# Performance work log

Measured on AMD Instinct MI355X. Metric: run time of the kernel, lower is better.

Reference implementation:

```python
import jax, jax.numpy as jnp
import numpy as np
import math

N_LEVELS = 4          # quadtree depth; leaves = 4**4 = 256
N_HEAD = 8
LN_EPS = 1e-5

def _tree_consts():
    # level d has 4**d nodes; offsets[d] = first node index of level d
    sizes = [4 ** d for d in range(N_LEVELS + 1)]
    offsets = np.concatenate([[0], np.cumsum(sizes)])
    n_nodes = int(offsets[-1])  # 341
    parent = np.full(n_nodes, -1, np.int64)
    for d in range(1, N_LEVELS + 1):
        idx = offsets[d] + np.arange(sizes[d])
        parent[idx] = offsets[d - 1] + np.arange(sizes[d]) // 4
    # chain[c, k] = k-th ancestor of c (k=0 -> self); padded by clamping at root
    chain = np.zeros((n_nodes, N_LEVELS + 1), np.int64)
    chain[:, 0] = np.arange(n_nodes)
    for k in range(1, N_LEVELS + 1):
        prev = chain[:, k - 1]
        chain[:, k] = np.where(parent[prev] >= 0, parent[prev], prev)
    nodes_at = [offsets[d] + np.arange(sizes[d]) for d in range(N_LEVELS + 1)]
    return chain, nodes_at, n_nodes

CHAIN, NODES_AT, N_NODES = _tree_consts()

def layernorm(x, g, b):
    m = jnp.mean(x, -1, keepdims=True)
    v = jnp.var(x, -1, keepdims=True)
    return (x - m) * jax.lax.rsqrt(v + LN_EPS) * g + b

def mhsa(x, w_qkv, b_qkv, w_proj, b_proj):
    B, N, E = x.shape
    hd = E // N_HEAD
    qkv = x @ w_qkv + b_qkv                       # (B, N, 3E)
    q, k, v = jnp.split(qkv, 3, axis=-1)
    sh = lambda t: t.reshape(B, N, N_HEAD, hd).transpose(0, 2, 1, 3)  # (B,H,N,hd)
    q, k, v = sh(q), sh(k), sh(v)
    att = jax.nn.softmax(jnp.einsum('bhqd,bhkd->bhqk', q, k) / math.sqrt(hd), axis=-1)
    o = jnp.einsum('bhqk,bhkd->bhqd', att, v).transpose(0, 2, 1, 3).reshape(B, N, E)
    return o @ w_proj + b_proj

def branch_mlp(x, M, b1, w2, b2):
    # Sparse equivalent of einsum('bni,bjmni->bmj', x, W1): W1[:, c, a, :]
    # is nonzero only for a in {c} U ancestors(c), with the weight matrix
    # depending only on (depth(c), depth(a)). Group nodes by depth and sum
    # over ancestor offsets k (depth(a) = d - k).
    B, N, E = x.shape
    h = jnp.zeros((B, N, 4 * E), x.dtype)
    for d in range(N_LEVELS + 1):
        nd = NODES_AT[d]                           # static numpy indices
        acc = jnp.zeros((B, nd.shape[0], 4 * E), x.dtype)
        for k in range(d + 1):
            src = CHAIN[nd, k]                     # ancestor at depth d-k
            acc = acc + jnp.einsum('bne,je->bnj', x[:, src, :], M[d, d - k])
        h = h.at[:, nd, :].set(acc)
    h = jax.nn.relu(h + b1[None, :, :])
    return h @ w2 + b2

def setup_inputs() -> dict:
    key = jax.random.key(0)
    ks = jax.random.split(key, 6)
    B, N, E = 64, N_NODES, 512
    s = 0.02
    return {
        'x': jax.random.normal(ks[0], (B, N, E), jnp.float32),
        'ln1_g': jnp.ones((E,), jnp.float32),
        'ln1_b': jnp.zeros((E,), jnp.float32),
        'w_qkv': jax.random.normal(ks[1], (E, 3 * E), jnp.float32) * s,
        'b_qkv': jnp.zeros((3 * E,), jnp.float32),
        'w_proj': jax.random.normal(ks[2], (E, E), jnp.float32) * s,
        'b_proj': jnp.zeros((E,), jnp.float32),
        'ln2_g': jnp.ones((E,), jnp.float32),
        'ln2_b': jnp.zeros((E,), jnp.float32),
        'mlp_M': jax.random.normal(ks[3], (N_LEVELS + 1, N_LEVELS + 1, 4 * E, E), jnp.float32) * s,
        'mlp_b1': jnp.zeros((N, 4 * E), jnp.float32),
        'w2': jax.random.normal(ks[4], (4 * E, E), jnp.float32) * s,
        'b2': jnp.zeros((E,), jnp.float32),
    }

def reference(x, ln1_g, ln1_b, w_qkv, b_qkv, w_proj, b_proj,
              ln2_g, ln2_b, mlp_M, mlp_b1, w2, b2):
    x = x + mhsa(layernorm(x, ln1_g, ln1_b), w_qkv, b_qkv, w_proj, b_proj)
    x = x + branch_mlp(layernorm(x, ln2_g, ln2_b), mlp_M, mlp_b1, w2, b2)
    return x
```

## Files before the change

kernel.cpp:

```cpp
#include <hip/hip_runtime.h>
#include <hip/hip_bf16.h>


typedef __attribute__((ext_vector_type(8))) __bf16 bf16x8;
typedef __attribute__((ext_vector_type(4))) float f32x4;
typedef __attribute__((ext_vector_type(4))) unsigned int u32x4;

#define GF_RELU    1
#define GF_OUTBF16 2

static __device__ __forceinline__ bf16x8 bzero8() {
    u32x4 z = {0u, 0u, 0u, 0u};
    return __builtin_bit_cast(bf16x8, z);
}

__global__ void transpose_bf16_kernel(const float* __restrict__ in,
                                      __hip_bfloat16* __restrict__ out,
                                      int K, int N, int log2K) {
    int idx = blockIdx.x * 256 + threadIdx.x;
    if (idx >= K * N) return;
    int n = idx >> log2K;
    int k = idx & (K - 1);
    out[idx] = __float2bfloat16(in[(size_t)k * N + n]);
}

__global__ void pack_wcat_kernel(const float* __restrict__ M,
                                 __hip_bfloat16* __restrict__ out) {
    int p = blockIdx.y;
    int s, d;
    if (p < 5)       { s = 0; d = p; }
    else if (p < 9)  { s = 1; d = p - 4; }
    else if (p < 12) { s = 2; d = p - 7; }
    else if (p < 14) { s = 3; d = p - 9; }
    else             { s = 4; d = 4; }
    const int base_lut[5] = {0, 5, 9, 12, 14};
    size_t idx = (size_t)blockIdx.x * 256 + threadIdx.x;
    const size_t MB = 2048ull * 512;
    out[(size_t)base_lut[s] * MB + (size_t)(d - s) * MB + idx] =
        __float2bfloat16(M[((size_t)d * 5 + s) * MB + idx]);
}

__global__ __launch_bounds__(256) void ln_kernel(const float* __restrict__ x,
                                                 const float* __restrict__ g,
                                                 const float* __restrict__ b,
                                                 __hip_bfloat16* __restrict__ out) {
    int tok = blockIdx.x;
    const float* xr = x + (size_t)tok * 512;
    int t = threadIdx.x;
    float v0 = xr[t], v1 = xr[t + 256];
    float s = v0 + v1;
    float s2 = v0 * v0 + v1 * v1;
    #pragma unroll
    for (int o = 32; o > 0; o >>= 1) {
        s  += __shfl_down(s, o);
        s2 += __shfl_down(s2, o);
    }
    __shared__ float ps[4], ps2[4];
    int w = t >> 6, lane = t & 63;
    if (lane == 0) { ps[w] = s; ps2[w] = s2; }
    __syncthreads();
    if (t == 0) {
        float ts = 0.f, ts2 = 0.f;
        #pragma unroll
        for (int i = 0; i < 4; i++) { ts += ps[i]; ts2 += ps2[i]; }
        ps[0] = ts * (1.f / 512.f);
        ps2[0] = ts2 * (1.f / 512.f);
    }
    __syncthreads();
    float m = ps[0];
    float var = ps2[0] - m * m;
    float r = rsqrtf(var + 1e-5f);
    out[(size_t)tok * 512 + t]       = __float2bfloat16((v0 - m) * r * g[t] + b[t]);
    out[(size_t)tok * 512 + t + 256] = __float2bfloat16((v1 - m) * r * g[t + 256] + b[t + 256]);
}

#define ATT_STR 72
__global__ __launch_bounds__(256) void attn_mfma_kernel(const __hip_bfloat16* __restrict__ qkv,
                                                        __hip_bfloat16* __restrict__ ctx) {
    __shared__ __bf16 kt_lds[64 * ATT_STR];
    __shared__ __bf16 vt_lds[64 * ATT_STR];
    __shared__ __bf16 pbuf[4 * 48 * ATT_STR];

    const int bh = blockIdx.x;
    const int half = blockIdx.y;
    const int b = bh >> 3, h = bh & 7;
    const int tid = threadIdx.x;
    const int w = tid >> 6, lane = tid & 63;
    const int q = lane >> 4, l16 = lane & 15;
    const int rowbase = half * 192 + w * 48;
    __bf16* pw = pbuf + w * 48 * ATT_STR;

    bf16x8 qf[3][2];
    #pragma unroll
    for (int mi = 0; mi < 3; mi++) {
        int row = rowbase + mi * 16 + l16;
        #pragma unroll
        for (int ks = 0; ks < 2; ks++) {
            if (row < 341)
                qf[mi][ks] = *(const bf16x8*)(qkv + (size_t)(b * 341 + row) * 1536 +
                                              h * 64 + ks * 32 + q * 8);
            else
                qf[mi][ks] = bzero8();
        }
    }

    f32x4 O[3][4];
    float mrun[3][4], lrun[3][4];
    #pragma unroll
    for (int mi = 0; mi < 3; mi++) {
        #pragma unroll
        for (int ni = 0; ni < 4; ni++) { f32x4 z = {0.f,0.f,0.f,0.f}; O[mi][ni] = z; }
        #pragma unroll
        for (int rr = 0; rr < 4; rr++) { mrun[mi][rr] = -1e30f; lrun[mi][rr] = 0.f; }
    }

    for (int kt6 = 0; kt6 < 6; kt6++) {
        const int kbase = kt6 * 64;
        __syncthreads();
        {
            int key = tid >> 2, kg = tid & 3;
            int gk = kbase + key;
            bf16x8 a0 = bzero8(), a1 = bzero8();
            if (gk < 341) {
                const __hip_bfloat16* src =
                    qkv + (size_t)(b * 341 + gk) * 1536 + 512 + h * 64 + kg * 16;
                a0 = *(const bf16x8*)src;
                a1 = *(const bf16x8*)(src + 8);
            }
            *(bf16x8*)(kt_lds + key * ATT_STR + kg * 16)     = a0;
            *(bf16x8*)(kt_lds + key * ATT_STR + kg * 16 + 8) = a1;
        }
        {
            int key = tid & 63, dg = tid >> 6;
            int gk = kbase + key;
            bf16x8 a0 = bzero8(), a1 = bzero8();
            if (gk < 341) {
                const __hip_bfloat16* src =
                    qkv + (size_t)(b * 341 + gk) * 1536 + 1024 + h * 64 + dg * 16;
                a0 = *(const bf16x8*)src;
                a1 = *(const bf16x8*)(src + 8);
            }
            #pragma unroll
            for (int j = 0; j < 8; j++) {
                vt_lds[(dg * 16 + j) * ATT_STR + key]     = a0[j];
                vt_lds[(dg * 16 + 8 + j) * ATT_STR + key] = a1[j];
            }
        }
        __syncthreads();

        f32x4 S[3][4];
        #pragma unroll
        for (int mi = 0; mi < 3; mi++)
            #pragma unroll
            for (int ni = 0; ni < 4; ni++) { f32x4 z = {0.f,0.f,0.f,0.f}; S[mi][ni] = z; }
        #pragma unroll
        for (int ks = 0; ks < 2; ks++) {
            bf16x8 bf_[4];
            #pragma unroll
            for (int ni = 0; ni < 4; ni++)
                bf_[ni] = *(const bf16x8*)(kt_lds + (ni * 16 + l16) * ATT_STR + ks * 32 + q * 8);
            #pragma unroll
            for (int mi = 0; mi < 3; mi++)
                #pragma unroll
                for (int ni = 0; ni < 4; ni++)
                    S[mi][ni] = __builtin_amdgcn_mfma_f32_16x16x32_bf16(qf[mi][ks], bf_[ni],
                                                                        S[mi][ni], 0, 0, 0);
        }

        float cmask[4];
        #pragma unroll
        for (int ni = 0; ni < 4; ni++)
            cmask[ni] = (kbase + ni * 16 + l16 < 341) ? 0.f : -1e30f;

        #pragma unroll
        for (int mi = 0; mi < 3; mi++) {
            #pragma unroll
            for (int rr = 0; rr < 4; rr++) {
                float rmax = -1e30f;
                #pragma unroll
                for (int ni = 0; ni < 4; ni++)
                    rmax = fmaxf(rmax, fmaf(S[mi][ni][rr], 0.125f, cmask[ni]));
                rmax = fmaxf(rmax, __shfl_xor(rmax, 1));
                rmax = fmaxf(rmax, __shfl_xor(rmax, 2));
                rmax = fmaxf(rmax, __shfl_xor(rmax, 4));
                rmax = fmaxf(rmax, __shfl_xor(rmax, 8));
                float mnew = fmaxf(mrun[mi][rr], rmax);
                float alpha = __expf(mrun[mi][rr] - mnew);
                mrun[mi][rr] = mnew;
                float psum = 0.f;
                #pragma unroll
                for (int ni = 0; ni < 4; ni++) {
                    float p = __expf(fmaf(S[mi][ni][rr], 0.125f, cmask[ni]) - mnew);
                    S[mi][ni][rr] = p;
                    psum += p;
                    O[mi][ni][rr] *= alpha;
                }
                psum += __shfl_xor(psum, 1);
                psum += __shfl_xor(psum, 2);
                psum += __shfl_xor(psum, 4);
                psum += __shfl_xor(psum, 8);
                lrun[mi][rr] = lrun[mi][rr] * alpha + psum;
            }
            #pragma unroll
            for (int ni = 0; ni < 4; ni++)
                #pragma unroll
                for (int rr = 0; rr < 4; rr++)
                    pw[(mi * 16 + q * 4 + rr) * ATT_STR + ni * 16 + l16] =
                        (__bf16)S[mi][ni][rr];
        }
        __syncthreads();

        #pragma unroll
        for (int ks = 0; ks < 2; ks++) {
            bf16x8 pf[3], vf[4];
            #pragma unroll
            for (int mi = 0; mi < 3; mi++)
                pf[mi] = *(const bf16x8*)(pw + (mi * 16 + l16) * ATT_STR + ks * 32 + q * 8);
            #pragma unroll
            for (int ni = 0; ni < 4; ni++)
                vf[ni] = *(const bf16x8*)(vt_lds + (ni * 16 + l16) * ATT_STR + ks * 32 + q * 8);
            #pragma unroll
            for (int mi = 0; mi < 3; mi++)
                #pragma unroll
                for (int ni = 0; ni < 4; ni++)
                    O[mi][ni] = __builtin_amdgcn_mfma_f32_16x16x32_bf16(pf[mi], vf[ni],
                                                                        O[mi][ni], 0, 0, 0);
        }
    }

    #pragma unroll
    for (int mi = 0; mi < 3; mi++) {
        #pragma unroll
        for (int rr = 0; rr < 4; rr++) {
            int row = rowbase + mi * 16 + q * 4 + rr;
            if (row >= 341) continue;
            float inv = 1.f / lrun[mi][rr];
            __hip_bfloat16* op = ctx + (size_t)(b * 341 + row) * 512 + h * 64;
            #pragma unroll
            for (int ni = 0; ni < 4; ni++)
                op[ni * 16 + l16] = __float2bfloat16(O[mi][ni][rr] * inv);
        }
    }
}

template <bool GATHER>
__global__ __launch_bounds__(256) void gemm_bf16(
    const __hip_bfloat16* __restrict__ A, const __hip_bfloat16* __restrict__ Bt,
    const float* __restrict__ bias, const float* __restrict__ resid,
    float* __restrict__ Cf, __hip_bfloat16* __restrict__ Cb,
    int Mrows, int N, int K, int flags, int depth) {
    __shared__ __hip_bfloat16 As[128 * 32];
    __shared__ __hip_bfloat16 Bs[128 * 32];
    const int tid = threadIdx.x;
    const int r = tid >> 1;
    const int kh = (tid & 1) << 4;
    const int gr = blockIdx.x * 128 + r;
    const int gn = blockIdx.y * 128 + r;
    const int lane = tid & 63;
    const int w = tid >> 6;
    const int wm = (w >> 1) << 6;
    const int wn = (w & 1) << 6;
    const int q = lane >> 4;
    const int l16 = lane & 15;

    size_t abase;
    if (GATHER) {
        const int dsh = depth << 1;
        const int bmask = (1 << dsh) - 1;
        int b = gr >> dsh;
        int i = gr & bmask;
        int node = (0x55555555 & bmask) + i;
        abase = ((size_t)(b * 341 + node)) << 9;
    } else {
        abase = (size_t)gr * K;
    }

    f32x4 acc[4][4];
    #pragma unroll
    for (int i = 0; i < 4; i++)
        #pragma unroll
        for (int j = 0; j < 4; j++) {
            f32x4 z = {0.f, 0.f, 0.f, 0.f};
            acc[i][j] = z;
        }

    for (int k0 = 0; k0 < K; k0 += 32) {
        bf16x8 va0 = bzero8(), va1 = bzero8(), vb0, vb1;
        if (gr < Mrows) {
            const bf16x8* p = (const bf16x8*)(A + abase + k0 + kh);
            va0 = p[0];
            va1 = p[1];
        }
        {
            const bf16x8* p = (const bf16x8*)(Bt + (size_t)gn * K + k0 + kh);
            vb0 = p[0];
            vb1 = p[1];
        }
        __syncthreads();
        *(bf16x8*)(As + r * 32 + kh)     = va0;
        *(bf16x8*)(As + r * 32 + kh + 8) = va1;
        *(bf16x8*)(Bs + r * 32 + kh)     = vb0;
        *(bf16x8*)(Bs + r * 32 + kh + 8) = vb1;
        __syncthreads();
        bf16x8 af[4], bfr[4];
        #pragma unroll
        for (int mi = 0; mi < 4; mi++)
            af[mi] = *(const bf16x8*)(As + (wm + mi * 16 + l16) * 32 + q * 8);
        #pragma unroll
        for (int ni = 0; ni < 4; ni++)
            bfr[ni] = *(const bf16x8*)(Bs + (wn + ni * 16 + l16) * 32 + q * 8);
        #pragma unroll
        for (int mi = 0; mi < 4; mi++)
            #pragma unroll
            for (int ni = 0; ni < 4; ni++)
                acc[mi][ni] = __builtin_amdgcn_mfma_f32_16x16x32_bf16(
                    af[mi], bfr[ni], acc[mi][ni], 0, 0, 0);
    }

    #pragma unroll
    for (int mi = 0; mi < 4; mi++) {
        #pragma unroll
        for (int rr = 0; rr < 4; rr++) {
            int grow = blockIdx.x * 128 + wm + mi * 16 + q * 4 + rr;
            if (grow >= Mrows) continue;
            size_t obase = (size_t)grow * N;
            #pragma unroll
            for (int ni = 0; ni < 4; ni++) {
                int col = blockIdx.y * 128 + wn + ni * 16 + l16;
                float v = acc[mi][ni][rr];
                if (bias) v += bias[col];
                if (resid) v += resid[obase + col];
                if (flags & GF_RELU) v = fmaxf(v, 0.f);
                if (flags & GF_OUTBF16)
                    Cb[obase + col] = __float2bfloat16(v);
                else
                    Cf[obase + col] = v;
            }
        }
    }
}

__global__ __launch_bounds__(256) void combine_kernel(const __hip_bfloat16* __restrict__ Y,
                                                      const float* __restrict__ b1,
                                                      __hip_bfloat16* __restrict__ h) {
    const size_t yoff[5] = {0, 655360, 2752512, 9043968, 25821184};
    int row = blockIdx.x;
    int b = row / 341;
    int node = row - b * 341;
    int d = (node >= 85) ? 4 : (node >= 21) ? 3 : (node >= 5) ? 2 : (node >= 1) ? 1 : 0;
    int i = node - (0x55555555 & ((1 << (d << 1)) - 1));
    int j = threadIdx.x << 3;

    float acc[8];
    const float* bp = b1 + (size_t)node * 2048 + j;
    f32x4 b0 = *(const f32x4*)bp;
    f32x4 b4 = *(const f32x4*)(bp + 4);
    #pragma unroll
    for (int u = 0; u < 4; u++) { acc[u] = b0[u]; acc[u + 4] = b4[u]; }

    #pragma unroll
    for (int s = 0; s < 5; s++) {
        if (s <= d) {
            int a = i >> ((d - s) << 1);
            int width = (5 - s) << 11;
            const bf16x8 v = *(const bf16x8*)(Y + yoff[s] +
                (size_t)((b << (s << 1)) + a) * width + ((d - s) << 11) + j);
            #pragma unroll
            for (int u = 0; u < 8; u++) acc[u] += (float)v[u];
        }
    }
    bf16x8 o;
    #pragma unroll
    for (int u = 0; u < 8; u++) o[u] = (__bf16)fmaxf(acc[u], 0.f);
    *(bf16x8*)(h + (size_t)row * 2048 + j) = o;
}

extern "C" void kernel_launch(void* const* d_in, const int* in_sizes, int n_in,
                              void* d_out, int out_size, void* d_ws, size_t ws_size,
                              hipStream_t stream) {
    const float* x      = (const float*)d_in[0];
    const float* ln1_g  = (const float*)d_in[1];
    const float* ln1_b  = (const float*)d_in[2];
    const float* w_qkv  = (const float*)d_in[3];
    const float* b_qkv  = (const float*)d_in[4];
    const float* w_proj = (const float*)d_in[5];
    const float* b_proj = (const float*)d_in[6];
    const float* ln2_g  = (const float*)d_in[7];
    const float* ln2_b  = (const float*)d_in[8];
    const float* mlp_M  = (const float*)d_in[9];
    const float* mlp_b1 = (const float*)d_in[10];
    const float* w2     = (const float*)d_in[11];
    const float* b2     = (const float*)d_in[12];
    float* out = (float*)d_out;

    const int M = 64 * 341;

    char* ws = (char*)d_ws;
    size_t off = 0;
    auto alloc = [&](size_t bytes) -> char* {
        char* p = ws + off;
        off += (bytes + 255) & ~(size_t)255;
        return p;
    };
    __hip_bfloat16* xn     = (__hip_bfloat16*)alloc((size_t)M * 512 * 2);
    __hip_bfloat16* wqkvT  = (__hip_bfloat16*)alloc(1536ull * 512 * 2);
    __hip_bfloat16* wprojT = (__hip_bfloat16*)alloc(512ull * 512 * 2);
    __hip_bfloat16* w2T    = (__hip_bfloat16*)alloc(512ull * 2048 * 2);
    __hip_bfloat16* wcat   = (__hip_bfloat16*)alloc(15ull * 2048 * 512 * 2);
    __hip_bfloat16* hbuf   = (__hip_bfloat16*)alloc((size_t)M * 2048 * 2);
    const size_t qkv_bytes = (size_t)M * 1536 * 2;
    const size_t y_bytes   = 59375616ull * 2;
    char* shared = alloc(y_bytes);
    __hip_bfloat16* qkv = (__hip_bfloat16*)shared;
    __hip_bfloat16* ctx = (__hip_bfloat16*)(shared + qkv_bytes);
    __hip_bfloat16* Y   = (__hip_bfloat16*)shared;
    if (off > ws_size) return;

    transpose_bf16_kernel<<<(512 * 1536 + 255) / 256, 256, 0, stream>>>(w_qkv, wqkvT, 512, 1536, 9);
    transpose_bf16_kernel<<<(512 * 512 + 255) / 256, 256, 0, stream>>>(w_proj, wprojT, 512, 512, 9);
    transpose_bf16_kernel<<<(2048 * 512 + 255) / 256, 256, 0, stream>>>(w2, w2T, 2048, 512, 11);
    pack_wcat_kernel<<<dim3(4096, 15), 256, 0, stream>>>(mlp_M, wcat);

    ln_kernel<<<M, 256, 0, stream>>>(x, ln1_g, ln1_b, xn);
    gemm_bf16<false><<<dim3((M + 127) / 128, 1536 / 128), 256, 0, stream>>>(
        xn, wqkvT, b_qkv, nullptr, nullptr, qkv, M, 1536, 512, GF_OUTBF16, 0);
    attn_mfma_kernel<<<dim3(512, 2), 256, 0, stream>>>(qkv, ctx);
    gemm_bf16<false><<<dim3((M + 127) / 128, 512 / 128), 256, 0, stream>>>(
        ctx, wprojT, b_proj, x, out, nullptr, M, 512, 512, 0, 0);

    ln_kernel<<<M, 256, 0, stream>>>(out, ln2_g, ln2_b, xn);
    const size_t yoff[5]     = {0, 655360, 2752512, 9043968, 25821184};
    const size_t wcat_off[5] = {0, 5, 9, 12, 14};
    for (int s = 0; s <= 4; s++) {
        int rows = 64 << (2 * s);
        int Ns = (5 - s) * 2048;
        gemm_bf16<true><<<dim3((rows + 127) / 128, Ns / 128), 256, 0, stream>>>(
            xn, wcat + wcat_off[s] * (2048ull * 512), nullptr, nullptr, nullptr,
            Y + yoff[s], rows, Ns, 512, GF_OUTBF16, s);
    }
    combine_kernel<<<M, 256, 0, stream>>>(Y, mlp_b1, hbuf);
    gemm_bf16<false><<<dim3((M + 127) / 128, 512 / 128), 256, 0, stream>>>(
        hbuf, w2T, b2, out, out, nullptr, M, 512, 2048, 0, 0);
}
```

Baseline: 858.0 us.

## Replace 128x128 GEMM with pipelined 256x256 LDS-DMA kernel with XCD remap

Replaces the simple register-staged 128x128 bf16 GEMM with a 256x256-tile, 512-thread kernel. It loads tiles directly into double-buffered, XOR-swizzled LDS using global_load_lds, and interleaves those loads with MFMA phases under explicit barriers and priority hints. A 1D grid with XCD-aware block remapping is meant to improve L2 locality. The goals are higher MFMA utilisation, fewer LDS bank conflicts and less global-load latency on all the GEMMs. The cost is 128KB of LDS per block and large tiles that may waste work on small-M gather stages, such as the 64-row depth-0 stage.

```diff
diff --git a/kernel.cpp b/kernel.cpp
--- a/kernel.cpp
+++ b/kernel.cpp
@@ -243,91 +243,198 @@
     }
 }
 
+__device__ __forceinline__ void gload16(const __hip_bfloat16* g, __bf16* l) {
+    __builtin_amdgcn_global_load_lds(
+        (const __attribute__((address_space(1))) void*)g,
+        (__attribute__((address_space(3))) void*)l, 16, 0, 0);
+}
+
+#define FULL_BAR() do { asm volatile("" ::: "memory");                        \
+    __builtin_amdgcn_sched_barrier(0);                                        \
+    __builtin_amdgcn_s_barrier();                                             \
+    __builtin_amdgcn_sched_barrier(0); } while (0)
+
+#define LGKM0() do {                                                          \
+    asm volatile("s_waitcnt lgkmcnt(0)" ::: "memory");                        \
+    __builtin_amdgcn_sched_barrier(0); } while (0)
+
+#define STAGE(arr, pr, isB, h, koff) do {                                     \
+    __bf16* _d = &smem[((((((pr) << 1) + (isB)) << 1) + (h)) << 13) + w * 1024]; \
+    gload16(arr[h][0] + (koff), _d);                                          \
+    gload16(arr[h][1] + (koff), _d + 512);                                    \
+} while (0)
+
 template <bool GATHER>
-__global__ __launch_bounds__(256) void gemm_bf16(
+__global__ __launch_bounds__(512, 2) void gemm256(
     const __hip_bfloat16* __restrict__ A, const __hip_bfloat16* __restrict__ Bt,
     const float* __restrict__ bias, const float* __restrict__ resid,
     float* __restrict__ Cf, __hip_bfloat16* __restrict__ Cb,
-    int Mrows, int N, int K, int flags, int depth) {
-    __shared__ __hip_bfloat16 As[128 * 32];
-    __shared__ __hip_bfloat16 Bs[128 * 32];
+    int Mrows, int N, int K, int flags, int depth, int gridN) {
+    __shared__ __align__(128) __bf16 smem[65536];
+
+    const int nwg = gridDim.x;
+    const int bid = blockIdx.x;
+    const int xcd = bid & 7, o = bid >> 3;
+    const int qq = nwg >> 3, rr = nwg & 7;
+    const int lin = (xcd < rr ? xcd * (qq + 1) : rr * (qq + 1) + (xcd - rr) * qq) + o;
+    const int bx = lin / gridN;
+    const int by = lin - bx * gridN;
+    const int bm0 = bx << 8, bn0 = by << 8;
+
     const int tid = threadIdx.x;
-    const int r = tid >> 1;
-    const int kh = (tid & 1) << 4;
-    const int gr = blockIdx.x * 128 + r;
-    const int gn = blockIdx.y * 128 + r;
-    const int lane = tid & 63;
-    const int w = tid >> 6;
-    const int wm = (w >> 1) << 6;
-    const int wn = (w & 1) << 6;
-    const int q = lane >> 4;
-    const int l16 = lane & 15;
-
-    size_t abase;
-    if (GATHER) {
-        const int dsh = depth << 1;
-        const int bmask = (1 << dsh) - 1;
-        int b = gr >> dsh;
-        int i = gr & bmask;
-        int node = (0x55555555 & bmask) + i;
-        abase = ((size_t)(b * 341 + node)) << 9;
-    } else {
-        abase = (size_t)gr * K;
-    }
-
-    f32x4 acc[4][4];
-    #pragma unroll
-    for (int i = 0; i < 4; i++)
+    const int w = tid >> 6, l = tid & 63;
+    const int l16 = l & 15, q = l >> 4;
+    const int wm = w >> 2, wn = w & 3;
+    const int lr8 = l >> 3;
+    const int slog = (l & 7) ^ lr8;
+
+    const __hip_bfloat16* aptr[2][2];
+    const __hip_bfloat16* bptr[2][2];
+    #pragma unroll
+    for (int h = 0; h < 2; h++)
+        #pragma unroll
+        for (int j = 0; j < 2; j++) {
+            int lr = (w * 2 + j) * 8 + lr8;
+            int grow = bm0 + h * 128 + lr;
+            if (grow > Mrows - 1) grow = Mrows - 1;
+            size_t abase;
+            if (GATHER) {
+                const int dsh = depth << 1;
+                const int bmask = (1 << dsh) - 1;
+                int bb = grow >> dsh;
+                int ii = grow & bmask;
+                int node = (0x55555555 & bmask) + ii;
+                abase = ((size_t)(bb * 341 + node)) << 9;
+            } else {
+                abase = (size_t)grow * K;
+            }
+            aptr[h][j] = A + abase + slog * 8;
+            bptr[h][j] = Bt + (size_t)(bn0 + h * 128 + lr) * K + slog * 8;
+        }
+
+    const int sl0 = ((q ^ (l16 & 7)) << 3);
+    const int sl1 = (((4 + q) ^ (l16 & 7)) << 3);
+
+    f32x4 acc[8][4];
+    #pragma unroll
+    for (int i = 0; i < 8; i++)
         #pragma unroll
         for (int j = 0; j < 4; j++) {
             f32x4 z = {0.f, 0.f, 0.f, 0.f};
             acc[i][j] = z;
         }
 
-    for (int k0 = 0; k0 < K; k0 += 32) {
-        bf16x8 va0 = bzero8(), va1 = bzero8(), vb0, vb1;
-        if (gr < Mrows) {
-            const bf16x8* p = (const bf16x8*)(A + abase + k0 + kh);
-            va0 = p[0];
-            va1 = p[1];
-        }
-        {
-            const bf16x8* p = (const bf16x8*)(Bt + (size_t)gn * K + k0 + kh);
-            vb0 = p[0];
-            vb1 = p[1];
-        }
-        __syncthreads();
-        *(bf16x8*)(As + r * 32 + kh)     = va0;
-        *(bf16x8*)(As + r * 32 + kh + 8) = va1;
-        *(bf16x8*)(Bs + r * 32 + kh)     = vb0;
-        *(bf16x8*)(Bs + r * 32 + kh + 8) = vb1;
-        __syncthreads();
-        bf16x8 af[4], bfr[4];
-        #pragma unroll
-        for (int mi = 0; mi < 4; mi++)
-            af[mi] = *(const bf16x8*)(As + (wm + mi * 16 + l16) * 32 + q * 8);
-        #pragma unroll
-        for (int ni = 0; ni < 4; ni++)
-            bfr[ni] = *(const bf16x8*)(Bs + (wn + ni * 16 + l16) * 32 + q * 8);
-        #pragma unroll
-        for (int mi = 0; mi < 4; mi++)
-            #pragma unroll
-            for (int ni = 0; ni < 4; ni++)
-                acc[mi][ni] = __builtin_amdgcn_mfma_f32_16x16x32_bf16(
-                    af[mi], bfr[ni], acc[mi][ni], 0, 0, 0);
-    }
-
-    #pragma unroll
-    for (int mi = 0; mi < 4; mi++) {
-        #pragma unroll
-        for (int rr = 0; rr < 4; rr++) {
-            int grow = blockIdx.x * 128 + wm + mi * 16 + q * 4 + rr;
+    STAGE(aptr, 0, 0, 0, 0);  STAGE(aptr, 0, 0, 1, 0);
+    STAGE(bptr, 0, 1, 0, 0);  STAGE(bptr, 0, 1, 1, 0);
+    STAGE(bptr, 1, 1, 0, 64); STAGE(bptr, 1, 1, 1, 64);
+    STAGE(aptr, 1, 0, 0, 64); STAGE(aptr, 1, 0, 1, 64);
+    asm volatile("s_waitcnt vmcnt(8)" ::: "memory");
+    __builtin_amdgcn_sched_barrier(0);
+    FULL_BAR();
+
+    const int NT = K >> 6;
+    bf16x8 af[4][2], b0[2][2], b1[2][2];
+
+    for (int t = 0; t < NT; ++t) {
+        const int p = t & 1;
+        const int aro = ((p << 2) + wm) << 13;
+        const int bro = ((((p << 1) + 1) << 1) + (wn >> 1)) * 8192 + ((wn & 1) << 12);
+
+        #pragma unroll
+        for (int mi = 0; mi < 4; mi++) {
+            af[mi][0] = *(const bf16x8*)&smem[aro + (mi * 16 + l16) * 64 + sl0];
+            af[mi][1] = *(const bf16x8*)&smem[aro + (mi * 16 + l16) * 64 + sl1];
+        }
+        #pragma unroll
+        for (int ni = 0; ni < 2; ni++) {
+            b0[ni][0] = *(const bf16x8*)&smem[bro + (ni * 16 + l16) * 64 + sl0];
+            b0[ni][1] = *(const bf16x8*)&smem[bro + (ni * 16 + l16) * 64 + sl1];
+        }
+        if (t >= 1 && t + 1 < NT) STAGE(aptr, (t + 1) & 1, 0, 0, (t + 1) << 6);
+        FULL_BAR();
+        LGKM0();
+        __builtin_amdgcn_s_setprio(1);
+        #pragma unroll
+        for (int ks = 0; ks < 2; ks++)
+            #pragma unroll
+            for (int mi = 0; mi < 4; mi++)
+                #pragma unroll
+                for (int ni = 0; ni < 2; ni++)
+                    acc[mi][ni] = __builtin_amdgcn_mfma_f32_16x16x32_bf16(
+                        af[mi][ks], b0[ni][ks], acc[mi][ni], 0, 0, 0);
+        __builtin_amdgcn_s_setprio(0);
+        FULL_BAR();
+
+        #pragma unroll
+        for (int ni = 0; ni < 2; ni++) {
+            b1[ni][0] = *(const bf16x8*)&smem[bro + ((ni + 2) * 16 + l16) * 64 + sl0];
+            b1[ni][1] = *(const bf16x8*)&smem[bro + ((ni + 2) * 16 + l16) * 64 + sl1];
+        }
+        if (t >= 1 && t + 1 < NT) STAGE(aptr, (t + 1) & 1, 0, 1, (t + 1) << 6);
+        FULL_BAR();
+        LGKM0();
+        __builtin_amdgcn_s_setprio(1);
+        #pragma unroll
+        for (int ks = 0; ks < 2; ks++)
+            #pragma unroll
+            for (int mi = 0; mi < 4; mi++)
+                #pragma unroll
+                for (int ni = 0; ni < 2; ni++)
+                    acc[mi][ni + 2] = __builtin_amdgcn_mfma_f32_16x16x32_bf16(
+                        af[mi][ks], b1[ni][ks], acc[mi][ni + 2], 0, 0, 0);
+        __builtin_amdgcn_s_setprio(0);
+        FULL_BAR();
+
+        #pragma unroll
+        for (int mi = 0; mi < 4; mi++) {
+            af[mi][0] = *(const bf16x8*)&smem[aro + ((mi + 4) * 16 + l16) * 64 + sl0];
+            af[mi][1] = *(const bf16x8*)&smem[aro + ((mi + 4) * 16 + l16) * 64 + sl1];
+        }
+        if (t + 2 < NT) STAGE(bptr, p, 1, 0, (t + 2) << 6);
+        FULL_BAR();
+        LGKM0();
+        __builtin_amdgcn_s_setprio(1);
+        #pragma unroll
+        for (int ks = 0; ks < 2; ks++)
+            #pragma unroll
+            for (int mi = 0; mi < 4; mi++)
+                #pragma unroll
+                for (int ni = 0; ni < 2; ni++)
+                    acc[mi + 4][ni + 2] = __builtin_amdgcn_mfma_f32_16x16x32_bf16(
+                        af[mi][ks], b1[ni][ks], acc[mi + 4][ni + 2], 0, 0, 0);
+        __builtin_amdgcn_s_setprio(0);
+        FULL_BAR();
+
+        if (t + 2 < NT) STAGE(bptr, p, 1, 1, (t + 2) << 6);
+        __builtin_amdgcn_s_setprio(1);
+        #pragma unroll
+        for (int ks = 0; ks < 2; ks++)
+            #pragma unroll
+            for (int mi = 0; mi < 4; mi++)
+                #pragma unroll
+                for (int ni = 0; ni < 2; ni++)
+                    acc[mi + 4][ni] = __builtin_amdgcn_mfma_f32_16x16x32_bf16(
+                        af[mi][ks], b0[ni][ks], acc[mi + 4][ni], 0, 0, 0);
+        __builtin_amdgcn_s_setprio(0);
+        if (t + 1 < NT) {
+            if (t + 2 < NT) { asm volatile("s_waitcnt vmcnt(4)" ::: "memory"); }
+            else            { asm volatile("s_waitcnt vmcnt(0)" ::: "memory"); }
+            __builtin_amdgcn_sched_barrier(0);
+        }
+        FULL_BAR();
+    }
+
+    #pragma unroll
+    for (int mi = 0; mi < 8; mi++) {
+        #pragma unroll
+        for (int rr2 = 0; rr2 < 4; rr2++) {
+            int grow = bm0 + wm * 128 + mi * 16 + q * 4 + rr2;
             if (grow >= Mrows) continue;
             size_t obase = (size_t)grow * N;
             #pragma unroll
             for (int ni = 0; ni < 4; ni++) {
-                int col = blockIdx.y * 128 + wn + ni * 16 + l16;
-                float v = acc[mi][ni][rr];
+                int col = bn0 + wn * 64 + ni * 16 + l16;
+                float v = acc[mi][ni][rr2];
                 if (bias) v += bias[col];
                 if (resid) v += resid[obase + col];
                 if (flags & GF_RELU) v = fmaxf(v, 0.f);
@@ -416,17 +523,27 @@
     __hip_bfloat16* Y   = (__hip_bfloat16*)shared;
     if (off > ws_size) return;
 
+    auto g256 = [&](bool gather, const __hip_bfloat16* A, const __hip_bfloat16* Bt,
+                    const float* bias, const float* resid, float* Cf,
+                    __hip_bfloat16* Cb, int Mr, int N, int K, int flags, int depth) {
+        int gm = (Mr + 255) >> 8, gn = N >> 8;
+        if (gather)
+            gemm256<true><<<dim3(gm * gn), 512, 0, stream>>>(
+                A, Bt, bias, resid, Cf, Cb, Mr, N, K, flags, depth, gn);
+        else
+            gemm256<false><<<dim3(gm * gn), 512, 0, stream>>>(
+                A, Bt, bias, resid, Cf, Cb, Mr, N, K, flags, depth, gn);
+    };
+
     transpose_bf16_kernel<<<(512 * 1536 + 255) / 256, 256, 0, stream>>>(w_qkv, wqkvT, 512, 1536, 9);
     transpose_bf16_kernel<<<(512 * 512 + 255) / 256, 256, 0, stream>>>(w_proj, wprojT, 512, 512, 9);
     transpose_bf16_kernel<<<(2048 * 512 + 255) / 256, 256, 0, stream>>>(w2, w2T, 2048, 512, 11);
     pack_wcat_kernel<<<dim3(4096, 15), 256, 0, stream>>>(mlp_M, wcat);
 
     ln_kernel<<<M, 256, 0, stream>>>(x, ln1_g, ln1_b, xn);
-    gemm_bf16<false><<<dim3((M + 127) / 128, 1536 / 128), 256, 0, stream>>>(
-        xn, wqkvT, b_qkv, nullptr, nullptr, qkv, M, 1536, 512, GF_OUTBF16, 0);
+    g256(false, xn, wqkvT, b_qkv, nullptr, nullptr, qkv, M, 1536, 512, GF_OUTBF16, 0);
     attn_mfma_kernel<<<dim3(512, 2), 256, 0, stream>>>(qkv, ctx);
-    gemm_bf16<false><<<dim3((M + 127) / 128, 512 / 128), 256, 0, stream>>>(
-        ctx, wprojT, b_proj, x, out, nullptr, M, 512, 512, 0, 0);
+    g256(false, ctx, wprojT, b_proj, x, out, nullptr, M, 512, 512, 0, 0);
 
     ln_kernel<<<M, 256, 0, stream>>>(out, ln2_g, ln2_b, xn);
     const size_t yoff[5]     = {0, 655360, 2752512, 9043968, 25821184};
@@ -434,11 +551,9 @@
     for (int s = 0; s <= 4; s++) {
         int rows = 64 << (2 * s);
         int Ns = (5 - s) * 2048;
-        gemm_bf16<true><<<dim3((rows + 127) / 128, Ns / 128), 256, 0, stream>>>(
-            xn, wcat + wcat_off[s] * (2048ull * 512), nullptr, nullptr, nullptr,
-            Y + yoff[s], rows, Ns, 512, GF_OUTBF16, s);
+        g256(true, xn, wcat + wcat_off[s] * (2048ull * 512), nullptr, nullptr, nullptr,
+             Y + yoff[s], rows, Ns, 512, GF_OUTBF16, s);
     }
     combine_kernel<<<M, 256, 0, stream>>>(Y, mlp_b1, hbuf);
-    gemm_bf16<false><<<dim3((M + 127) / 128, 512 / 128), 256, 0, stream>>>(
-        hbuf, w2T, b2, out, out, nullptr, M, 512, 2048, 0, 0);
-}
+    g256(false, hbuf, w2T, b2, out, out, nullptr, M, 512, 2048, 0, 0);
+}
```

After: 918.7 us. +7.1%, slower.

## Fuse per-depth branch GEMMs into one launch and remap blocks across XCDs

Applied to the files above, without the earlier changes.

The five per-depth branch GEMM launches become a single grouped GEMM kernel. It uses a flat grid and picks the depth segment from the linear block index, so small depth-0/1 GEMMs no longer run as separate under-filled launches. All GEMMs now use a 1D grid with an XCD-aware block remap, so consecutive tiles sharing A/B rows land on the same XCD and its L2. This adds integer division and branching per block, and the block-to-tile ordering changes.

```diff
diff --git a/kernel.cpp b/kernel.cpp
--- a/kernel.cpp
+++ b/kernel.cpp
@@ -244,18 +244,17 @@
 }
 
 template <bool GATHER>
-__global__ __launch_bounds__(256) void gemm_bf16(
+static __device__ __forceinline__ void gemm128_body(
+    __hip_bfloat16* As, __hip_bfloat16* Bs,
     const __hip_bfloat16* __restrict__ A, const __hip_bfloat16* __restrict__ Bt,
     const float* __restrict__ bias, const float* __restrict__ resid,
     float* __restrict__ Cf, __hip_bfloat16* __restrict__ Cb,
-    int Mrows, int N, int K, int flags, int depth) {
-    __shared__ __hip_bfloat16 As[128 * 32];
-    __shared__ __hip_bfloat16 Bs[128 * 32];
+    int Mrows, int N, int K, int flags, int depth, int bm0, int bn0) {
     const int tid = threadIdx.x;
     const int r = tid >> 1;
     const int kh = (tid & 1) << 4;
-    const int gr = blockIdx.x * 128 + r;
-    const int gn = blockIdx.y * 128 + r;
+    const int gr = bm0 + r;
+    const int gn = bn0 + r;
     const int lane = tid & 63;
     const int w = tid >> 6;
     const int wm = (w >> 1) << 6;
@@ -321,12 +320,12 @@
     for (int mi = 0; mi < 4; mi++) {
         #pragma unroll
         for (int rr = 0; rr < 4; rr++) {
-            int grow = blockIdx.x * 128 + wm + mi * 16 + q * 4 + rr;
+            int grow = bm0 + wm + mi * 16 + q * 4 + rr;
             if (grow >= Mrows) continue;
             size_t obase = (size_t)grow * N;
             #pragma unroll
             for (int ni = 0; ni < 4; ni++) {
-                int col = blockIdx.y * 128 + wn + ni * 16 + l16;
+                int col = bn0 + wn + ni * 16 + l16;
                 float v = acc[mi][ni][rr];
                 if (bias) v += bias[col];
                 if (resid) v += resid[obase + col];
@@ -338,6 +337,53 @@
             }
         }
     }
+}
+
+static __device__ __forceinline__ int xcd_remap(int bid, int nwg) {
+    const int xcd = bid & 7, o = bid >> 3;
+    const int qq = nwg >> 3, rr = nwg & 7;
+    return (xcd < rr ? xcd * (qq + 1) : rr * (qq + 1) + (xcd - rr) * qq) + o;
+}
+
+__global__ __launch_bounds__(256) void gemm128(
+    const __hip_bfloat16* __restrict__ A, const __hip_bfloat16* __restrict__ Bt,
+    const float* __restrict__ bias, const float* __restrict__ resid,
+    float* __restrict__ Cf, __hip_bfloat16* __restrict__ Cb,
+    int Mrows, int N, int K, int flags, int gridN) {
+    __shared__ __hip_bfloat16 As[128 * 32];
+    __shared__ __hip_bfloat16 Bs[128 * 32];
+    const int lin = xcd_remap(blockIdx.x, gridDim.x);
+    const int bx = lin / gridN;
+    const int by = lin - bx * gridN;
+    gemm128_body<false>(As, Bs, A, Bt, bias, resid, Cf, Cb,
+                        Mrows, N, K, flags, 0, bx << 7, by << 7);
+}
+
+__global__ __launch_bounds__(256) void gemm_branch_fused(
+    const __hip_bfloat16* __restrict__ xn, const __hip_bfloat16* __restrict__ wcat,
+    __hip_bfloat16* __restrict__ Y) {
+    __shared__ __hip_bfloat16 As[128 * 32];
+    __shared__ __hip_bfloat16 Bs[128 * 32];
+    const int lin = xcd_remap(blockIdx.x, gridDim.x);
+    int s;
+    if (lin < 80)        s = 0;
+    else if (lin < 208)  s = 1;
+    else if (lin < 592)  s = 2;
+    else if (lin < 1616) s = 3;
+    else                 s = 4;
+    const int base_tab[5] = {0, 80, 208, 592, 1616};
+    const int gn_tab[5]   = {80, 64, 48, 32, 16};
+    const size_t yoff[5]  = {0, 655360, 2752512, 9043968, 25821184};
+    const int wcat_off[5] = {0, 5, 9, 12, 14};
+    const int loc = lin - base_tab[s];
+    const int gn = gn_tab[s];
+    const int bx = loc / gn;
+    const int by = loc - bx * gn;
+    const int Mrows = 64 << (s << 1);
+    const int N = (5 - s) << 11;
+    gemm128_body<true>(As, Bs, xn, wcat + (size_t)wcat_off[s] * (2048ull * 512),
+                       nullptr, nullptr, nullptr, Y + yoff[s],
+                       Mrows, N, 512, GF_OUTBF16, s, bx << 7, by << 7);
 }
 
 __global__ __launch_bounds__(256) void combine_kernel(const __hip_bfloat16* __restrict__ Y,
@@ -416,29 +462,26 @@
     __hip_bfloat16* Y   = (__hip_bfloat16*)shared;
     if (off > ws_size) return;
 
+    auto g128 = [&](const __hip_bfloat16* A, const __hip_bfloat16* Bt,
+                    const float* bias, const float* resid, float* Cf,
+                    __hip_bfloat16* Cb, int Mr, int N, int K, int flags) {
+        int gm = (Mr + 127) >> 7, gn = N >> 7;
+        gemm128<<<dim3(gm * gn), 256, 0, stream>>>(
+            A, Bt, bias, resid, Cf, Cb, Mr, N, K, flags, gn);
+    };
+
     transpose_bf16_kernel<<<(512 * 1536 + 255) / 256, 256, 0, stream>>>(w_qkv, wqkvT, 512, 1536, 9);
     transpose_bf16_kernel<<<(512 * 512 + 255) / 256, 256, 0, stream>>>(w_proj, wprojT, 512, 512, 9);
     transpose_bf16_kernel<<<(2048 * 512 + 255) / 256, 256, 0, stream>>>(w2, w2T, 2048, 512, 11);
     pack_wcat_kernel<<<dim3(4096, 15), 256, 0, stream>>>(mlp_M, wcat);
 
     ln_kernel<<<M, 256, 0, stream>>>(x, ln1_g, ln1_b, xn);
-    gemm_bf16<false><<<dim3((M + 127) / 128, 1536 / 128), 256, 0, stream>>>(
-        xn, wqkvT, b_qkv, nullptr, nullptr, qkv, M, 1536, 512, GF_OUTBF16, 0);
+    g128(xn, wqkvT, b_qkv, nullptr, nullptr, qkv, M, 1536, 512, GF_OUTBF16);
     attn_mfma_kernel<<<dim3(512, 2), 256, 0, stream>>>(qkv, ctx);
-    gemm_bf16<false><<<dim3((M + 127) / 128, 512 / 128), 256, 0, stream>>>(
-        ctx, wprojT, b_proj, x, out, nullptr, M, 512, 512, 0, 0);
+    g128(ctx, wprojT, b_proj, x, out, nullptr, M, 512, 512, 0);
 
     ln_kernel<<<M, 256, 0, stream>>>(out, ln2_g, ln2_b, xn);
-    const size_t yoff[5]     = {0, 655360, 2752512, 9043968, 25821184};
-    const size_t wcat_off[5] = {0, 5, 9, 12, 14};
-    for (int s = 0; s <= 4; s++) {
-        int rows = 64 << (2 * s);
-        int Ns = (5 - s) * 2048;
-        gemm_bf16<true><<<dim3((rows + 127) / 128, Ns / 128), 256, 0, stream>>>(
-            xn, wcat + wcat_off[s] * (2048ull * 512), nullptr, nullptr, nullptr,
-            Y + yoff[s], rows, Ns, 512, GF_OUTBF16, s);
-    }
+    gemm_branch_fused<<<dim3(3664), 256, 0, stream>>>(xn, wcat, Y);
     combine_kernel<<<M, 256, 0, stream>>>(Y, mlp_b1, hbuf);
-    gemm_bf16<false><<<dim3((M + 127) / 128, 512 / 128), 256, 0, stream>>>(
-        hbuf, w2T, b2, out, out, nullptr, M, 512, 2048, 0, 0);
-}
+    g128(hbuf, w2T, b2, out, out, nullptr, M, 512, 2048, 0);
+}
```

New measurement: 785.3 us. 8.5% less time.
